# Optimization experiments

Measured on AMD Instinct MI355X. Metric: run time of the kernel, lower is better.

The kernel has to match this reference:

```python
import jax, jax.numpy as jnp
import numpy as np

N, E, C, NE, G, T = 20000, 320000, 32, 10, 64, 1000
NB, HID, LAYERS = 8, 64, 2
R_MAX, P_CUT, AVG_NEIGH = 5.0, 6, 16.0
LM = 16  # (max_ell+1)^2 spherical-harmonic components
L_OF_LM = jnp.array([0,1,1,1,2,2,2,2,2,3,3,3,3,3,3,3])


def sph_harm(u):
    # component-normalized real spherical harmonics up to l=3 on unit vectors u [E,3]
    x, y, z = u[:, 0], u[:, 1], u[:, 2]
    s3, s15, s5, s105, s7 = 3**0.5, 15**0.5, 5**0.5, 105**0.5, 7**0.5
    s35_8, s21_8 = (35.0/8.0)**0.5, (21.0/8.0)**0.5
    comps = [jnp.ones_like(x),
             s3*x, s3*y, s3*z,
             s15*x*y, s15*y*z, 0.5*s5*(3*z*z-1.0), s15*x*z, 0.5*s15*(x*x-y*y),
             s35_8*y*(3*x*x-y*y), s105*x*y*z, s21_8*y*(5*z*z-1.0),
             0.5*s7*(5*z*z*z-3*z), s21_8*x*(5*z*z-1.0),
             0.5*s105*z*(x*x-y*y), s35_8*x*(x*x-3*y*y)]
    return jnp.stack(comps, axis=-1)  # [E,16]


def radial_embed(r):
    # Bessel basis with polynomial cutoff (MACE RadialEmbeddingBlock)
    n = jnp.arange(1, NB + 1, dtype=r.dtype)
    rc = jnp.maximum(r, 1e-9)
    bessel = (2.0/R_MAX)**0.5 * jnp.sin(n[None, :]*jnp.pi*rc[:, None]/R_MAX) / rc[:, None]
    xr = r / R_MAX
    p = float(P_CUT)
    f = (1.0 - 0.5*(p+1)*(p+2)*xr**p + p*(p+2)*xr**(p+1) - 0.5*p*(p+1)*xr**(p+2))
    f = f * (xr < 1.0)
    return bessel * f[:, None]  # [E,NB]


def setup_inputs():
    key = jax.random.key(0)
    ks = jax.random.split(key, 16)
    positions = jax.random.normal(ks[0], (N, 3)) * 3.0
    species = jax.random.randint(ks[1], (N,), 0, NE)
    node_attrs = jax.nn.one_hot(species, NE, dtype=jnp.float32)
    edge_index = jax.random.randint(ks[2], (2, E), 0, N)
    shifts = jnp.zeros((E, 3), jnp.float32)
    batch = jnp.sort(jax.random.randint(ks[3], (N,), 0, G))
    t = jax.random.randint(ks[4], (G,), 0, T)
    eps = jax.random.normal(ks[5], (N, NE + 3))
    betas = jnp.linspace(1e-4, 0.02, T)
    alpha_bar = jnp.cumprod(1.0 - betas)
    sc = 0.1
    W_embed = sc * jax.random.normal(ks[6], (NE + 1, C))
    W_r1 = sc * jax.random.normal(ks[7], (LAYERS, NB, HID))
    W_r2 = sc * jax.random.normal(ks[8], (LAYERS, HID, C * 4))
    W_mix = sc * jax.random.normal(ks[9], (LAYERS, 4, C, C))
    W_sc = sc * jax.random.normal(ks[10], (NE, C))
    W_prod = sc * jax.random.normal(ks[11], (LAYERS, 3, C))
    W_ro_s = sc * jax.random.normal(ks[12], (LAYERS, C, NE))
    W_ro_v = sc * jax.random.normal(ks[13], (LAYERS, C))
    return {"positions": positions, "node_attrs": node_attrs, "shifts": shifts,
            "eps": eps, "alpha_bar": alpha_bar, "W_embed": W_embed, "W_r1": W_r1,
            "W_r2": W_r2, "W_mix": W_mix, "W_sc": W_sc, "W_prod": W_prod,
            "W_ro_s": W_ro_s, "W_ro_v": W_ro_v, "edge_index": edge_index,
            "batch": batch, "t": t}


def reference(positions, node_attrs, shifts, eps, alpha_bar, W_embed, W_r1, W_r2,
              W_mix, W_sc, W_prod, W_ro_s, W_ro_v, edge_index, batch, t):
    sender, receiver = edge_index[0], edge_index[1]
    # diffusion: noise positions and attrs (DDPM q(x_t|x_0))
    ab = alpha_bar[t][batch][:, None]                       # [N,1]
    attrs0 = node_attrs / 4.0
    pos_noisy = jnp.sqrt(ab) * positions + jnp.sqrt(1.0 - ab) * eps[:, -3:]
    attrs_noisy = jnp.sqrt(ab) * attrs0 + jnp.sqrt(1.0 - ab) * eps[:, :NE]
    tf = (t.astype(jnp.float32) / T)[batch][:, None]
    h = jnp.concatenate([attrs_noisy, tf], axis=-1) @ W_embed  # [N,C]
    # edge geometry
    vec = pos_noisy[receiver] - pos_noisy[sender] + shifts
    r = jnp.sqrt(jnp.sum(vec * vec, axis=-1) + 1e-12)
    Y = sph_harm(vec / r[:, None])                          # [E,16]
    ef = radial_embed(r)                                    # [E,NB]
    scalar = h
    pred = jnp.zeros((N, NE + 3), h.dtype)
    for layer in range(LAYERS):
        rw = jax.nn.silu(ef @ W_r1[layer]) @ W_r2[layer]    # [E,4C]
        rw = rw.reshape(E, C, 4)[:, :, L_OF_LM]             # [E,C,16]
        msg = rw * scalar[sender][:, :, None] * Y[:, None, :]
        agg = jax.ops.segment_sum(msg, receiver, num_segments=N) / AVG_NEIGH
        Wm = W_mix[layer][L_OF_LM]                          # [16,C,C]
        feats = jnp.einsum('nck,kcd->ndk', agg, Wm)         # per-l channel mix
        s = feats[:, :, 0]
        poly = W_prod[layer, 0] + W_prod[layer, 1] * s + W_prod[layer, 2] * s * s
        feats = feats * poly[:, :, None]                    # correlation-3 product
        if layer == 0:
            feats = feats.at[:, :, 0].add(attrs_noisy @ W_sc)  # element skip
        scalar = feats[:, :, 0]
        pred_s = scalar @ W_ro_s[layer]                     # [N,NE]
        pred_v = jnp.einsum('ncm,c->nm', feats[:, :, 1:4], W_ro_v[layer])  # [N,3]
        pred = pred + jnp.concatenate([pred_s, pred_v], axis=-1)
    err = (pred - eps) ** 2
    loss_pos = jax.ops.segment_sum(err[:, -3:].sum(-1), batch, num_segments=G)
    loss_lab = jax.ops.segment_sum(err[:, :NE].sum(-1), batch, num_segments=G)
    nn = jax.ops.segment_sum(jnp.ones((N,), pred.dtype), batch, num_segments=G)
    loss = 0.5 * (loss_pos + loss_lab) / (jnp.maximum(nn, 1.0) * (3 + NE))
    return loss
```

## Files before the change

### kernel.cpp

```cpp
#include <hip/hip_runtime.h>

typedef unsigned short ushort_t;
typedef unsigned int uint_t;

#define NN 20000
#define EE 320000
#define CC 32
#define NEL 10
#define GG 64
#define TTT 1000
#define NBB 8
#define HIDD 64
#define NPB 4
#define MAXDEG 64

typedef __attribute__((ext_vector_type(8))) short bf16x8;
typedef __attribute__((ext_vector_type(4))) float f32x4;

__device__ __forceinline__ float bits2f(uint_t b) { union { uint_t u; float f; } v; v.u = b; return v.f; }
__device__ __forceinline__ ushort_t f2b(float f) {
  union { float f; uint_t u; } v; v.f = f;
  uint_t r = (v.u + 0x7fffu + ((v.u >> 16) & 1u)) >> 16;
  return (ushort_t)r;
}
__device__ __forceinline__ uint_t pk(float a, float b) {
  return (uint_t)f2b(a) | ((uint_t)f2b(b) << 16);
}
__device__ __forceinline__ float lo16(uint_t u) { return bits2f(u << 16); }
__device__ __forceinline__ float hi16(uint_t u) { return bits2f(u & 0xffff0000u); }

__global__ __launch_bounds__(256) void k_prep(
    const float* __restrict__ positions, const float* __restrict__ node_attrs,
    const float* __restrict__ eps, const float* __restrict__ alpha_bar,
    const float* __restrict__ W_embed, const float* __restrict__ W_sc,
    const int* __restrict__ batch, const int* __restrict__ tarr,
    float* __restrict__ pos_noisy, float* __restrict__ scalA,
    float* __restrict__ sc_skip, float* __restrict__ pred, int* __restrict__ deg)
{
  int n = blockIdx.x * 256 + threadIdx.x;
  if (n >= NN) return;
  deg[n] = 0;
  int g = batch[n];
  int tn = tarr[g];
  float ab = alpha_bar[tn];
  float sa = sqrtf(ab), sb = sqrtf(fmaxf(1.0f - ab, 0.0f));
#pragma unroll
  for (int j = 0; j < 3; ++j)
    pos_noisy[n * 3 + j] = sa * positions[n * 3 + j] + sb * eps[n * 13 + 10 + j];
  float an[10];
#pragma unroll
  for (int j = 0; j < 10; ++j)
    an[j] = sa * 0.25f * node_attrs[n * 10 + j] + sb * eps[n * 13 + j];
  float tf = (float)tn * (1.0f / (float)TTT);
  for (int d = 0; d < CC; ++d) {
    float h = tf * W_embed[10 * CC + d];
    float sk = 0.0f;
#pragma unroll
    for (int j = 0; j < 10; ++j) {
      h = fmaf(an[j], W_embed[j * CC + d], h);
      sk = fmaf(an[j], W_sc[j * CC + d], sk);
    }
    scalA[n * CC + d] = h;
    sc_skip[n * CC + d] = sk;
  }
#pragma unroll
  for (int j = 0; j < 13; ++j) pred[n * 13 + j] = 0.0f;
}

__global__ __launch_bounds__(256) void k_edge_deg(const int* __restrict__ ei,
    int* __restrict__ deg)
{
  int e = blockIdx.x * 256 + threadIdx.x;
  atomicAdd(&deg[ei[EE + e]], 1);
}

__global__ __launch_bounds__(1024) void k_scan(const int* __restrict__ deg,
    int* __restrict__ offs, int* __restrict__ cursor,
    float* __restrict__ lnum, float* __restrict__ lcnt, int* __restrict__ ticket)
{
  __shared__ int wsums[16];
  __shared__ int woffs[16];
  int tid = threadIdx.x, lane = tid & 63, wv = tid >> 6;
  if (tid < GG) { lnum[tid] = 0.0f; lcnt[tid] = 0.0f; }
  if (tid == 1022) *ticket = 0;
  int base = tid * 20;
  int loc[20];
  int s = 0;
#pragma unroll
  for (int j = 0; j < 20; ++j) {
    int idx = base + j;
    int v = (idx < NN) ? deg[idx] : 0;
    loc[j] = s; s += v;
  }
  int inc = s;
  for (int o = 1; o < 64; o <<= 1) {
    int v = __shfl_up(inc, o, 64);
    if (lane >= o) inc += v;
  }
  if (lane == 63) wsums[wv] = inc;
  __syncthreads();
  if (wv == 0 && lane < 16) {
    int v = wsums[lane];
    int i2 = v;
    for (int o = 1; o < 16; o <<= 1) {
      int vv = __shfl_up(i2, o, 16);
      if (lane >= o) i2 += vv;
    }
    woffs[lane] = i2 - v;
  }
  __syncthreads();
  int texcl = woffs[wv] + (inc - s);
#pragma unroll
  for (int j = 0; j < 20; ++j) {
    int idx = base + j;
    if (idx < NN) { int v = texcl + loc[j]; offs[idx] = v; cursor[idx] = v; }
  }
  if (tid == 1023) offs[NN] = EE;
}

__global__ __launch_bounds__(256) void k_edge2(
    const float* __restrict__ pos_noisy, const float* __restrict__ shifts,
    const int* __restrict__ ei, int* __restrict__ cursor,
    ushort_t* __restrict__ Ys, ushort_t* __restrict__ efs, int* __restrict__ snds)
{
  int e = blockIdx.x * 256 + threadIdx.x;
  int snd = ei[e], rcv = ei[EE + e];
  float vx = pos_noisy[rcv * 3 + 0] - pos_noisy[snd * 3 + 0] + shifts[e * 3 + 0];
  float vy = pos_noisy[rcv * 3 + 1] - pos_noisy[snd * 3 + 1] + shifts[e * 3 + 1];
  float vz = pos_noisy[rcv * 3 + 2] - pos_noisy[snd * 3 + 2] + shifts[e * 3 + 2];
  float r2 = vx * vx + vy * vy + vz * vz + 1e-12f;
  float r = sqrtf(r2);
  float inv = 1.0f / r;
  float x = vx * inv, y = vy * inv, z = vz * inv;

  const float s3 = 1.7320508075688772f, s15 = 3.872983346207417f, s5 = 2.23606797749979f;
  const float s105 = 10.246950765959598f, s7 = 2.6457513110645907f;
  const float s35_8 = 2.091650066335189f, s21_8 = 1.6201851746019651f;
  float yv[16];
  yv[0] = 1.0f;
  yv[1] = s3 * x; yv[2] = s3 * y; yv[3] = s3 * z;
  yv[4] = s15 * x * y;
  yv[5] = s15 * y * z;
  yv[6] = 0.5f * s5 * (3.0f * z * z - 1.0f);
  yv[7] = s15 * x * z;
  yv[8] = 0.5f * s15 * (x * x - y * y);
  yv[9] = s35_8 * y * (3.0f * x * x - y * y);
  yv[10] = s105 * x * y * z;
  yv[11] = s21_8 * y * (5.0f * z * z - 1.0f);
  yv[12] = 0.5f * s7 * (5.0f * z * z * z - 3.0f * z);
  yv[13] = s21_8 * x * (5.0f * z * z - 1.0f);
  yv[14] = 0.5f * s105 * z * (x * x - y * y);
  yv[15] = s35_8 * x * (x * x - 3.0f * y * y);

  float rc = fmaxf(r, 1e-9f);
  float pref = 0.6324555320336759f / rc;
  float th = 0.6283185307179586f * rc;
  float s1 = __sinf(th), c1 = __cosf(th);
  float xr = r * 0.2f;
  float fcut = 0.0f;
  if (xr < 1.0f) {
    float x2 = xr * xr, x3 = x2 * xr;
    float x6 = x3 * x3, x7 = x6 * xr, x8 = x7 * xr;
    fcut = 1.0f - 28.0f * x6 + 48.0f * x7 - 21.0f * x8;
  }
  float efv[8];
  float sp = 0.0f, scur = s1, c2 = 2.0f * c1;
#pragma unroll
  for (int b = 0; b < 8; ++b) {
    efv[b] = pref * scur * fcut;
    float nx = c2 * scur - sp;
    sp = scur; scur = nx;
  }

  int slot = atomicAdd(&cursor[rcv], 1);
  snds[slot] = snd;
  uint4* Y4 = (uint4*)Ys;
  Y4[(size_t)slot * 2 + 0] = make_uint4(pk(yv[0], yv[1]), pk(yv[2], yv[3]),
                                        pk(yv[4], yv[5]), pk(yv[6], yv[7]));
  Y4[(size_t)slot * 2 + 1] = make_uint4(pk(yv[8], yv[9]), pk(yv[10], yv[11]),
                                        pk(yv[12], yv[13]), pk(yv[14], yv[15]));
  ((uint4*)efs)[slot] = make_uint4(pk(efv[0], efv[1]), pk(efv[2], efv[3]),
                                   pk(efv[4], efv[5]), pk(efv[6], efv[7]));
}

__global__ __launch_bounds__(256) void k_flay(
    const ushort_t* __restrict__ efs, const ushort_t* __restrict__ Ys,
    const int* __restrict__ snds, const int* __restrict__ offs,
    const float* __restrict__ W_r1, const float* __restrict__ W_r2,
    const float* __restrict__ scal_in, float* __restrict__ scal_out,
    const float* __restrict__ W_mix, const float* __restrict__ W_prod,
    const float* __restrict__ W_ro_s, const float* __restrict__ W_ro_v,
    const float* __restrict__ sc_skip, float* __restrict__ pred, int layer)
{
  __shared__ __align__(16) char lds[37376];
  ushort_t (*w2t)[72] = (ushort_t(*)[72])lds;
  float (*lagg)[CC][16] = (float(*)[CC][16])lds;
  float (*lf)[CC][4] = (float(*)[CC][4])(lds + 8192);
  float* w1s = (float*)(lds + 18432);

  int tid = threadIdx.x;
  int w = tid >> 6, lane = tid & 63;
  ushort_t (*rwt)[132] = (ushort_t(*)[132])(lds + 20480 + w * 4224);

  int n0 = blockIdx.x * NPB;
  const float* W1g = W_r1 + layer * NBB * HIDD;
  const float* W2g = W_r2 + layer * HIDD * 128;

  for (int idx = tid; idx < HIDD * 128; idx += 256) {
    int k = idx >> 7, n = idx & 127;
    w2t[n][k] = f2b(W2g[idx]);
  }
  for (int idx = tid; idx < NBB * HIDD; idx += 256) w1s[idx] = W1g[idx];
  __syncthreads();

  int c16 = lane & 15, quad = lane >> 4;
  bf16x8 bfr[16];
#pragma unroll
  for (int nt = 0; nt < 8; ++nt)
#pragma unroll
    for (int kt = 0; kt < 2; ++kt)
      bfr[nt * 2 + kt] = *(const bf16x8*)&w2t[nt * 16 + c16][kt * 32 + quad * 8];

  int oj = offs[n0 + w];
  int dj = min(offs[n0 + w + 1] - oj, MAXDEG);

  int cA = lane >> 1, kh = lane & 1, kb = kh * 8;
  float acc0 = 0, acc1 = 0, acc2 = 0, acc3 = 0, acc4 = 0, acc5 = 0, acc6 = 0, acc7 = 0;
  const uint4* Y4 = (const uint4*)Ys;

  for (int kbase = 0; kbase < dj; kbase += 16) {
    bf16x8 a0, a1;
    {
      int kc = kbase + c16;
      float ef8[8] = {0, 0, 0, 0, 0, 0, 0, 0};
      if (kc < dj) {
        uint4 q = ((const uint4*)efs)[(size_t)(oj + kc)];
        ef8[0] = lo16(q.x); ef8[1] = hi16(q.x); ef8[2] = lo16(q.y); ef8[3] = hi16(q.y);
        ef8[4] = lo16(q.z); ef8[5] = hi16(q.z); ef8[6] = lo16(q.w); ef8[7] = hi16(q.w);
      }
      float h0[8] = {0, 0, 0, 0, 0, 0, 0, 0};
      float h1v[8] = {0, 0, 0, 0, 0, 0, 0, 0};
#pragma unroll
      for (int b = 0; b < 8; ++b) {
        const float* wb = &w1s[b * HIDD];
        float4 wa = *(const float4*)&wb[quad * 8];
        float4 wbv = *(const float4*)&wb[quad * 8 + 4];
        float4 wc = *(const float4*)&wb[32 + quad * 8];
        float4 wd = *(const float4*)&wb[32 + quad * 8 + 4];
        float e = ef8[b];
        h0[0] = fmaf(e, wa.x, h0[0]); h0[1] = fmaf(e, wa.y, h0[1]);
        h0[2] = fmaf(e, wa.z, h0[2]); h0[3] = fmaf(e, wa.w, h0[3]);
        h0[4] = fmaf(e, wbv.x, h0[4]); h0[5] = fmaf(e, wbv.y, h0[5]);
        h0[6] = fmaf(e, wbv.z, h0[6]); h0[7] = fmaf(e, wbv.w, h0[7]);
        h1v[0] = fmaf(e, wc.x, h1v[0]); h1v[1] = fmaf(e, wc.y, h1v[1]);
        h1v[2] = fmaf(e, wc.z, h1v[2]); h1v[3] = fmaf(e, wc.w, h1v[3]);
        h1v[4] = fmaf(e, wd.x, h1v[4]); h1v[5] = fmaf(e, wd.y, h1v[5]);
        h1v[6] = fmaf(e, wd.z, h1v[6]); h1v[7] = fmaf(e, wd.w, h1v[7]);
      }
#pragma unroll
      for (int jj = 0; jj < 8; ++jj) {
        float v0 = h0[jj];  v0 = v0 / (1.0f + __expf(-v0));
        float v1 = h1v[jj]; v1 = v1 / (1.0f + __expf(-v1));
        a0[jj] = (short)f2b(v0);
        a1[jj] = (short)f2b(v1);
      }
    }
    int snd_[4];
#pragma unroll
    for (int r = 0; r < 4; ++r) {
      int kr = kbase + quad * 4 + r;
      snd_[r] = snds[oj + ((kr < dj) ? kr : (dj - 1))];
    }
#pragma unroll
    for (int nt = 0; nt < 8; ++nt) {
      f32x4 acc = {0.0f, 0.0f, 0.0f, 0.0f};
      acc = __builtin_amdgcn_mfma_f32_16x16x32_bf16(a0, bfr[nt * 2 + 0], acc, 0, 0, 0);
      acc = __builtin_amdgcn_mfma_f32_16x16x32_bf16(a1, bfr[nt * 2 + 1], acc, 0, 0, 0);
      int cc = 4 * nt + (c16 >> 2);
#pragma unroll
      for (int r = 0; r < 4; ++r)
        rwt[quad * 4 + r][nt * 16 + c16] = f2b(acc[r] * scal_in[(size_t)snd_[r] * CC + cc]);
    }
    asm volatile("s_waitcnt lgkmcnt(0)" ::: "memory");
    int emax = min(16, dj - kbase);
    for (int e = 0; e < emax; ++e) {
      size_t ge = (size_t)(oj + kbase + e);
      uint4 q = Y4[ge * 2 + kh];
      uint2 rp = *(const uint2*)&rwt[e][cA * 4];
      float r0 = lo16(rp.x), r1 = hi16(rp.x), r2v = lo16(rp.y), r3 = hi16(rp.y);
      float w0 = kh ? r2v : r0, w13 = kh ? r3 : r1, w47 = kh ? r3 : r2v;
      acc0 = fmaf(w0,  lo16(q.x), acc0);
      acc1 = fmaf(w13, hi16(q.x), acc1);
      acc2 = fmaf(w13, lo16(q.y), acc2);
      acc3 = fmaf(w13, hi16(q.y), acc3);
      acc4 = fmaf(w47, lo16(q.z), acc4);
      acc5 = fmaf(w47, hi16(q.z), acc5);
      acc6 = fmaf(w47, lo16(q.w), acc6);
      acc7 = fmaf(w47, hi16(q.w), acc7);
    }
  }
  __syncthreads();

  const float invavg = 1.0f / 16.0f;
  lagg[w][cA][kb + 0] = acc0 * invavg;
  lagg[w][cA][kb + 1] = acc1 * invavg;
  lagg[w][cA][kb + 2] = acc2 * invavg;
  lagg[w][cA][kb + 3] = acc3 * invavg;
  lagg[w][cA][kb + 4] = acc4 * invavg;
  lagg[w][cA][kb + 5] = acc5 * invavg;
  lagg[w][cA][kb + 6] = acc6 * invavg;
  lagg[w][cA][kb + 7] = acc7 * invavg;
  __syncthreads();

  int d = cA;
  int n = n0 + w;
  float ft[8] = {0, 0, 0, 0, 0, 0, 0, 0};
  const float* Wm = W_mix + layer * 4096;
  for (int cc2 = 0; cc2 < CC; ++cc2) {
    float m0 = Wm[cc2 * CC + d];
    float m1 = Wm[1024 + cc2 * CC + d];
    float m2 = Wm[2048 + cc2 * CC + d];
    float m3 = Wm[3072 + cc2 * CC + d];
    float u0 = kh ? m2 : m0;
    float u13 = kh ? m3 : m1;
    float u47 = kh ? m3 : m2;
    ft[0] = fmaf(lagg[w][cc2][kb + 0], u0, ft[0]);
    ft[1] = fmaf(lagg[w][cc2][kb + 1], u13, ft[1]);
    ft[2] = fmaf(lagg[w][cc2][kb + 2], u13, ft[2]);
    ft[3] = fmaf(lagg[w][cc2][kb + 3], u13, ft[3]);
    ft[4] = fmaf(lagg[w][cc2][kb + 4], u47, ft[4]);
    ft[5] = fmaf(lagg[w][cc2][kb + 5], u47, ft[5]);
    ft[6] = fmaf(lagg[w][cc2][kb + 6], u47, ft[6]);
    ft[7] = fmaf(lagg[w][cc2][kb + 7], u47, ft[7]);
  }
  float sv = __shfl(ft[0], lane & 62, 64);
  const float* Wp = W_prod + layer * 96;
  float p0 = Wp[d], p1 = Wp[32 + d], p2 = Wp[64 + d];
  float poly = fmaf(fmaf(p2, sv, p1), sv, p0);
#pragma unroll
  for (int j = 0; j < 8; ++j) ft[j] *= poly;
  if (layer == 0 && kh == 0) ft[0] += sc_skip[n * CC + d];
  if (kh == 0) {
    scal_out[n * CC + d] = ft[0];
    lf[w][d][0] = ft[0]; lf[w][d][1] = ft[1]; lf[w][d][2] = ft[2]; lf[w][d][3] = ft[3];
  }
  __syncthreads();
  if (lane < 13) {
    float sum = 0.0f;
    if (lane < 10) {
      const float* Wr = W_ro_s + layer * CC * NEL;
      for (int dd = 0; dd < CC; ++dd) sum = fmaf(lf[w][dd][0], Wr[dd * NEL + lane], sum);
    } else {
      int mm = lane - 10;
      const float* Wv = W_ro_v + layer * CC;
      for (int dd = 0; dd < CC; ++dd) sum = fmaf(lf[w][dd][1 + mm], Wv[dd], sum);
    }
    pred[n * 13 + lane] += sum;
  }
}

__global__ __launch_bounds__(256) void k_loss(const float* __restrict__ pred,
    const float* __restrict__ eps, const int* __restrict__ batch,
    float* __restrict__ lnum, float* __restrict__ lcnt,
    int* __restrict__ ticket, float* __restrict__ out, int nblocks)
{
  __shared__ float psum[GG];
  __shared__ int pcnt[GG];
  __shared__ int lastflag;
  int tid = threadIdx.x;
  if (tid < GG) { psum[tid] = 0.0f; pcnt[tid] = 0; }
  __syncthreads();
  int n = blockIdx.x * 256 + tid;
  if (n < NN) {
    int g = batch[n];
    float sum = 0.0f;
#pragma unroll
    for (int j = 0; j < 13; ++j) {
      float dlt = pred[n * 13 + j] - eps[n * 13 + j];
      sum = fmaf(dlt, dlt, sum);
    }
    atomicAdd(&psum[g], sum);
    atomicAdd(&pcnt[g], 1);
  }
  __syncthreads();
  if (tid < GG && pcnt[tid] > 0) {
    atomicAdd(&lnum[tid], psum[tid]);
    atomicAdd(&lcnt[tid], (float)pcnt[tid]);
  }
  __syncthreads();
  if (tid == 0) {
    __threadfence();
    int t = atomicAdd(ticket, 1);
    lastflag = (t == nblocks - 1) ? 1 : 0;
  }
  __syncthreads();
  if (lastflag && tid < GG) {
    float num = atomicAdd(&lnum[tid], 0.0f);
    float cnt = atomicAdd(&lcnt[tid], 0.0f);
    out[tid] = 0.5f * num / (fmaxf(cnt, 1.0f) * 13.0f);
  }
}

extern "C" void kernel_launch(void* const* d_in, const int* in_sizes, int n_in,
                              void* d_out, int out_size, void* d_ws, size_t ws_size,
                              hipStream_t stream) {
  const float* positions  = (const float*)d_in[0];
  const float* node_attrs = (const float*)d_in[1];
  const float* shifts     = (const float*)d_in[2];
  const float* eps        = (const float*)d_in[3];
  const float* alpha_bar  = (const float*)d_in[4];
  const float* W_embed    = (const float*)d_in[5];
  const float* W_r1       = (const float*)d_in[6];
  const float* W_r2       = (const float*)d_in[7];
  const float* W_mix      = (const float*)d_in[8];
  const float* W_sc       = (const float*)d_in[9];
  const float* W_prod     = (const float*)d_in[10];
  const float* W_ro_s     = (const float*)d_in[11];
  const float* W_ro_v     = (const float*)d_in[12];
  const int* edge_index   = (const int*)d_in[13];
  const int* batch        = (const int*)d_in[14];
  const int* tarr         = (const int*)d_in[15];
  float* out = (float*)d_out;

  char* ws = (char*)d_ws;
  size_t off = 0;
  auto alloc = [&](size_t bytes) -> void* {
    void* p = ws + off;
    off = (off + bytes + 255) & ~(size_t)255;
    return p;
  };
  float* pos_noisy = (float*)alloc(NN * 3 * 4);
  float* scalA     = (float*)alloc(NN * CC * 4);
  float* scalB     = (float*)alloc(NN * CC * 4);
  float* sc_skip   = (float*)alloc(NN * CC * 4);
  float* pred      = (float*)alloc(NN * 13 * 4);
  ushort_t* Ys     = (ushort_t*)alloc((size_t)EE * 16 * 2);
  ushort_t* efs    = (ushort_t*)alloc((size_t)EE * 8 * 2);
  int* snds        = (int*)alloc((size_t)EE * 4);
  int* deg         = (int*)alloc(NN * 4);
  int* offs        = (int*)alloc((NN + 1) * 4);
  int* cursor      = (int*)alloc(NN * 4);
  float* lnum      = (float*)alloc(GG * 4);
  float* lcnt      = (float*)alloc(GG * 4);
  int* ticket      = (int*)alloc(4);
  (void)ws_size; (void)in_sizes; (void)n_in; (void)out_size;

  const int NB_N = (NN + 255) / 256;
  const int NB_E = EE / 256;

  k_prep<<<NB_N, 256, 0, stream>>>(positions, node_attrs, eps, alpha_bar, W_embed,
                                   W_sc, batch, tarr, pos_noisy, scalA, sc_skip, pred, deg);
  k_edge_deg<<<NB_E, 256, 0, stream>>>(edge_index, deg);
  k_scan<<<1, 1024, 0, stream>>>(deg, offs, cursor, lnum, lcnt, ticket);
  k_edge2<<<NB_E, 256, 0, stream>>>(pos_noisy, shifts, edge_index, cursor, Ys, efs, snds);

  for (int layer = 0; layer < 2; ++layer) {
    const float* sin_p = (layer == 0) ? scalA : scalB;
    float* sout_p      = (layer == 0) ? scalB : scalA;
    k_flay<<<NN / NPB, 256, 0, stream>>>(efs, Ys, snds, offs, W_r1, W_r2,
                                         sin_p, sout_p, W_mix, W_prod,
                                         W_ro_s, W_ro_v, sc_skip, pred, layer);
  }

  k_loss<<<NB_N, 256, 0, stream>>>(pred, eps, batch, lnum, lcnt, ticket, out, NB_N);
}
```

Before: 366.9 us.

## Fuse degree histogram, scan and node prep; stage Y in LDS in layer kernel

Merges the node prep, edge-degree count and prefix scan into one launch. Block 0 builds the degree histogram in LDS, using packed 16-bit counters and shared-memory atomics, then scans it, while the other blocks do the node prep. In the layer kernel, the spherical-harmonic rows for each 16-edge tile are staged into LDS with one load per edge. The MFMA operands are swapped so each lane needs only one sender index and 8 scalar loads, and it writes packed uint2 values to LDS. The aim is fewer launches, no global atomics and fewer redundant global gathers. The risk is that a single block serially processes all 320k edges for the histogram, and 16-bit counters could overflow on high-degree nodes.

Result: slower. 431.5 us (+17.6%).

```diff
diff --git a/kernel.cpp b/kernel.cpp
--- a/kernel.cpp
+++ b/kernel.cpp
@@ -29,93 +29,96 @@
 __device__ __forceinline__ float lo16(uint_t u) { return bits2f(u << 16); }
 __device__ __forceinline__ float hi16(uint_t u) { return bits2f(u & 0xffff0000u); }
 
-__global__ __launch_bounds__(256) void k_prep(
+__global__ __launch_bounds__(1024) void k_scanprep(
     const float* __restrict__ positions, const float* __restrict__ node_attrs,
     const float* __restrict__ eps, const float* __restrict__ alpha_bar,
     const float* __restrict__ W_embed, const float* __restrict__ W_sc,
     const int* __restrict__ batch, const int* __restrict__ tarr,
+    const int* __restrict__ ei,
     float* __restrict__ pos_noisy, float* __restrict__ scalA,
-    float* __restrict__ sc_skip, float* __restrict__ pred, int* __restrict__ deg)
-{
-  int n = blockIdx.x * 256 + threadIdx.x;
-  if (n >= NN) return;
-  deg[n] = 0;
-  int g = batch[n];
-  int tn = tarr[g];
-  float ab = alpha_bar[tn];
-  float sa = sqrtf(ab), sb = sqrtf(fmaxf(1.0f - ab, 0.0f));
-#pragma unroll
-  for (int j = 0; j < 3; ++j)
-    pos_noisy[n * 3 + j] = sa * positions[n * 3 + j] + sb * eps[n * 13 + 10 + j];
-  float an[10];
-#pragma unroll
-  for (int j = 0; j < 10; ++j)
-    an[j] = sa * 0.25f * node_attrs[n * 10 + j] + sb * eps[n * 13 + j];
-  float tf = (float)tn * (1.0f / (float)TTT);
-  for (int d = 0; d < CC; ++d) {
-    float h = tf * W_embed[10 * CC + d];
-    float sk = 0.0f;
-#pragma unroll
-    for (int j = 0; j < 10; ++j) {
-      h = fmaf(an[j], W_embed[j * CC + d], h);
-      sk = fmaf(an[j], W_sc[j * CC + d], sk);
-    }
-    scalA[n * CC + d] = h;
-    sc_skip[n * CC + d] = sk;
-  }
-#pragma unroll
-  for (int j = 0; j < 13; ++j) pred[n * 13 + j] = 0.0f;
-}
-
-__global__ __launch_bounds__(256) void k_edge_deg(const int* __restrict__ ei,
-    int* __restrict__ deg)
-{
-  int e = blockIdx.x * 256 + threadIdx.x;
-  atomicAdd(&deg[ei[EE + e]], 1);
-}
-
-__global__ __launch_bounds__(1024) void k_scan(const int* __restrict__ deg,
+    float* __restrict__ sc_skip, float* __restrict__ pred,
     int* __restrict__ offs, int* __restrict__ cursor,
     float* __restrict__ lnum, float* __restrict__ lcnt, int* __restrict__ ticket)
 {
+  __shared__ uint_t hist[NN / 2];
   __shared__ int wsums[16];
   __shared__ int woffs[16];
-  int tid = threadIdx.x, lane = tid & 63, wv = tid >> 6;
-  if (tid < GG) { lnum[tid] = 0.0f; lcnt[tid] = 0.0f; }
-  if (tid == 1022) *ticket = 0;
-  int base = tid * 20;
-  int loc[20];
-  int s = 0;
-#pragma unroll
-  for (int j = 0; j < 20; ++j) {
-    int idx = base + j;
-    int v = (idx < NN) ? deg[idx] : 0;
-    loc[j] = s; s += v;
-  }
-  int inc = s;
-  for (int o = 1; o < 64; o <<= 1) {
-    int v = __shfl_up(inc, o, 64);
-    if (lane >= o) inc += v;
-  }
-  if (lane == 63) wsums[wv] = inc;
-  __syncthreads();
-  if (wv == 0 && lane < 16) {
-    int v = wsums[lane];
-    int i2 = v;
-    for (int o = 1; o < 16; o <<= 1) {
-      int vv = __shfl_up(i2, o, 16);
-      if (lane >= o) i2 += vv;
-    }
-    woffs[lane] = i2 - v;
-  }
-  __syncthreads();
-  int texcl = woffs[wv] + (inc - s);
-#pragma unroll
-  for (int j = 0; j < 20; ++j) {
-    int idx = base + j;
-    if (idx < NN) { int v = texcl + loc[j]; offs[idx] = v; cursor[idx] = v; }
-  }
-  if (tid == 1023) offs[NN] = EE;
+  int tid = threadIdx.x;
+  if (blockIdx.x == 0) {
+    int lane = tid & 63, wv = tid >> 6;
+    if (tid < GG) { lnum[tid] = 0.0f; lcnt[tid] = 0.0f; }
+    if (tid == 64) *ticket = 0;
+    for (int i = tid; i < NN / 2; i += 1024) hist[i] = 0u;
+    __syncthreads();
+#pragma unroll 4
+    for (int e = tid; e < EE; e += 1024) {
+      int r = ei[EE + e];
+      atomicAdd(&hist[r >> 1], 1u << ((r & 1) * 16));
+    }
+    __syncthreads();
+    int base = tid * 20;
+    int loc[20];
+    int s = 0;
+#pragma unroll
+    for (int j = 0; j < 20; ++j) {
+      int idx = base + j;
+      int v = 0;
+      if (idx < NN) v = (int)((hist[idx >> 1] >> ((idx & 1) * 16)) & 0xffffu);
+      loc[j] = s; s += v;
+    }
+    int inc = s;
+    for (int o = 1; o < 64; o <<= 1) {
+      int v = __shfl_up(inc, o, 64);
+      if (lane >= o) inc += v;
+    }
+    if (lane == 63) wsums[wv] = inc;
+    __syncthreads();
+    if (wv == 0 && lane < 16) {
+      int v = wsums[lane];
+      int i2 = v;
+      for (int o = 1; o < 16; o <<= 1) {
+        int vv = __shfl_up(i2, o, 16);
+        if (lane >= o) i2 += vv;
+      }
+      woffs[lane] = i2 - v;
+    }
+    __syncthreads();
+    int texcl = woffs[wv] + (inc - s);
+#pragma unroll
+    for (int j = 0; j < 20; ++j) {
+      int idx = base + j;
+      if (idx < NN) { int v = texcl + loc[j]; offs[idx] = v; cursor[idx] = v; }
+    }
+    if (tid == 1023) offs[NN] = EE;
+  } else {
+    int n = (blockIdx.x - 1) * 1024 + tid;
+    if (n >= NN) return;
+    int g = batch[n];
+    int tn = tarr[g];
+    float ab = alpha_bar[tn];
+    float sa = sqrtf(ab), sb = sqrtf(fmaxf(1.0f - ab, 0.0f));
+#pragma unroll
+    for (int j = 0; j < 3; ++j)
+      pos_noisy[n * 3 + j] = sa * positions[n * 3 + j] + sb * eps[n * 13 + 10 + j];
+    float an[10];
+#pragma unroll
+    for (int j = 0; j < 10; ++j)
+      an[j] = sa * 0.25f * node_attrs[n * 10 + j] + sb * eps[n * 13 + j];
+    float tf = (float)tn * (1.0f / (float)TTT);
+    for (int d = 0; d < CC; ++d) {
+      float h = tf * W_embed[10 * CC + d];
+      float sk = 0.0f;
+#pragma unroll
+      for (int j = 0; j < 10; ++j) {
+        h = fmaf(an[j], W_embed[j * CC + d], h);
+        sk = fmaf(an[j], W_sc[j * CC + d], sk);
+      }
+      scalA[n * CC + d] = h;
+      sc_skip[n * CC + d] = sk;
+    }
+#pragma unroll
+    for (int j = 0; j < 13; ++j) pred[n * 13 + j] = 0.0f;
+  }
 }
 
 __global__ __launch_bounds__(256) void k_edge2(
@@ -192,7 +195,7 @@
     const float* __restrict__ W_ro_s, const float* __restrict__ W_ro_v,
     const float* __restrict__ sc_skip, float* __restrict__ pred, int layer)
 {
-  __shared__ __align__(16) char lds[37376];
+  __shared__ __align__(16) char lds[39424];
   ushort_t (*w2t)[72] = (ushort_t(*)[72])lds;
   float (*lagg)[CC][16] = (float(*)[CC][16])lds;
   float (*lf)[CC][4] = (float(*)[CC][4])(lds + 8192);
@@ -201,6 +204,7 @@
   int tid = threadIdx.x;
   int w = tid >> 6, lane = tid & 63;
   ushort_t (*rwt)[132] = (ushort_t(*)[132])(lds + 20480 + w * 4224);
+  ushort_t (*ysh)[16] = (ushort_t(*)[16])(lds + 37376 + w * 512);
 
   int n0 = blockIdx.x * NPB;
   const float* W1g = W_r1 + layer * NBB * HIDD;
@@ -229,6 +233,13 @@
   const uint4* Y4 = (const uint4*)Ys;
 
   for (int kbase = 0; kbase < dj; kbase += 16) {
+    if (lane < 32) {
+      int et = lane >> 1, half = lane & 1;
+      int ke = kbase + et;
+      uint4 yq = make_uint4(0, 0, 0, 0);
+      if (ke < dj) yq = Y4[(size_t)(oj + ke) * 2 + half];
+      *(uint4*)&ysh[et][half * 8] = yq;
+    }
     bf16x8 a0, a1;
     {
       int kc = kbase + c16;
@@ -265,27 +276,29 @@
         a1[jj] = (short)f2b(v1);
       }
     }
-    int snd_[4];
-#pragma unroll
-    for (int r = 0; r < 4; ++r) {
-      int kr = kbase + quad * 4 + r;
-      snd_[r] = snds[oj + ((kr < dj) ? kr : (dj - 1))];
+    int kc = kbase + c16;
+    int snd_c = snds[oj + ((kc < dj) ? kc : (dj - 1))];
+    float ssv[8];
+    {
+      const float* sb = scal_in + (size_t)snd_c * CC + quad;
+#pragma unroll
+      for (int nt = 0; nt < 8; ++nt) ssv[nt] = sb[nt * 4];
     }
 #pragma unroll
     for (int nt = 0; nt < 8; ++nt) {
       f32x4 acc = {0.0f, 0.0f, 0.0f, 0.0f};
-      acc = __builtin_amdgcn_mfma_f32_16x16x32_bf16(a0, bfr[nt * 2 + 0], acc, 0, 0, 0);
-      acc = __builtin_amdgcn_mfma_f32_16x16x32_bf16(a1, bfr[nt * 2 + 1], acc, 0, 0, 0);
-      int cc = 4 * nt + (c16 >> 2);
-#pragma unroll
-      for (int r = 0; r < 4; ++r)
-        rwt[quad * 4 + r][nt * 16 + c16] = f2b(acc[r] * scal_in[(size_t)snd_[r] * CC + cc]);
+      acc = __builtin_amdgcn_mfma_f32_16x16x32_bf16(bfr[nt * 2 + 0], a0, acc, 0, 0, 0);
+      acc = __builtin_amdgcn_mfma_f32_16x16x32_bf16(bfr[nt * 2 + 1], a1, acc, 0, 0, 0);
+      float s = ssv[nt];
+      uint2 pw;
+      pw.x = pk(acc[0] * s, acc[1] * s);
+      pw.y = pk(acc[2] * s, acc[3] * s);
+      *(uint2*)&rwt[c16][nt * 16 + quad * 4] = pw;
     }
     asm volatile("s_waitcnt lgkmcnt(0)" ::: "memory");
     int emax = min(16, dj - kbase);
     for (int e = 0; e < emax; ++e) {
-      size_t ge = (size_t)(oj + kbase + e);
-      uint4 q = Y4[ge * 2 + kh];
+      uint4 q = *(const uint4*)&ysh[e][kh * 8];
       uint2 rp = *(const uint2*)&rwt[e][cA * 4];
       float r0 = lo16(rp.x), r1 = hi16(rp.x), r2v = lo16(rp.y), r3 = hi16(rp.y);
       float w0 = kh ? r2v : r0, w13 = kh ? r3 : r1, w47 = kh ? r3 : r2v;
@@ -437,7 +450,6 @@
   ushort_t* Ys     = (ushort_t*)alloc((size_t)EE * 16 * 2);
   ushort_t* efs    = (ushort_t*)alloc((size_t)EE * 8 * 2);
   int* snds        = (int*)alloc((size_t)EE * 4);
-  int* deg         = (int*)alloc(NN * 4);
   int* offs        = (int*)alloc((NN + 1) * 4);
   int* cursor      = (int*)alloc(NN * 4);
   float* lnum      = (float*)alloc(GG * 4);
@@ -447,11 +459,12 @@
 
   const int NB_N = (NN + 255) / 256;
   const int NB_E = EE / 256;
-
-  k_prep<<<NB_N, 256, 0, stream>>>(positions, node_attrs, eps, alpha_bar, W_embed,
-                                   W_sc, batch, tarr, pos_noisy, scalA, sc_skip, pred, deg);
-  k_edge_deg<<<NB_E, 256, 0, stream>>>(edge_index, deg);
-  k_scan<<<1, 1024, 0, stream>>>(deg, offs, cursor, lnum, lcnt, ticket);
+  const int NB_SP = 1 + (NN + 1023) / 1024;
+
+  k_scanprep<<<NB_SP, 1024, 0, stream>>>(positions, node_attrs, eps, alpha_bar,
+                                         W_embed, W_sc, batch, tarr, edge_index,
+                                         pos_noisy, scalA, sc_skip, pred,
+                                         offs, cursor, lnum, lcnt, ticket);
   k_edge2<<<NB_E, 256, 0, stream>>>(pos_noisy, shifts, edge_index, cursor, Ys, efs, snds);
 
   for (int layer = 0; layer < 2; ++layer) {
```
